# Kernel optimization log

Hardware: AMD Instinct MI355X
Metric: run time of the kernel (lower is better)

The kernel has to match this reference:

```python
import jax, jax.numpy as jnp
import numpy as np

B, T, H = 65536, 34, 64
T10_LO, T10_HI = 0.1, 5.0
M0_LO, M0_HI = 0.0, 10000.0


def setup_inputs() -> dict:
    key = jax.random.key(0)
    ks = jax.random.split(key, 24)
    sig = jax.random.uniform(ks[0], (B, T), jnp.float32, 0.1, 1.0)
    keep = jax.random.uniform(ks[1], (B, T)) > 0.3
    X_fa_in = jnp.where(keep, sig, 0.0)
    fa_vals = jax.random.uniform(ks[2], (B, T), jnp.float32, 0.05, 0.6)  # flip angles (rad)
    fa_mask = keep
    fa_len = jnp.sum(keep, axis=1).astype(jnp.int64)
    TR_vals = jax.random.uniform(ks[3], (B, 1), jnp.float32, 0.003, 0.01)
    gi = 1.0 / np.sqrt(H)
    p = {}
    p['gru_Wih'] = jax.random.uniform(ks[4], (3 * H, 2), jnp.float32, -gi, gi)
    p['gru_Whh'] = jax.random.uniform(ks[5], (3 * H, H), jnp.float32, -gi, gi)
    p['gru_bih'] = jax.random.uniform(ks[6], (3 * H,), jnp.float32, -gi, gi)
    p['gru_bhh'] = jax.random.uniform(ks[7], (3 * H,), jnp.float32, -gi, gi)
    p['score_T10_w'] = jax.random.normal(ks[8], (H,), jnp.float32) * gi
    p['score_M0_w'] = jax.random.normal(ks[9], (H,), jnp.float32) * gi
    def lin(kw, kb, fan_out, fan_in):
        b = 1.0 / np.sqrt(fan_in)
        return (jax.random.uniform(kw, (fan_out, fan_in), jnp.float32, -b, b),
                jax.random.uniform(kb, (fan_out,), jnp.float32, -b, b))
    p['regT_W1'], p['regT_b1'] = lin(ks[10], ks[11], 200, H)
    p['regT_W2'], p['regT_b2'] = lin(ks[12], ks[13], 200, 200)
    p['regT_W3'], p['regT_b3'] = lin(ks[14], ks[15], 1, 200)
    p['regM_W1'], p['regM_b1'] = lin(ks[16], ks[17], 200, H)
    p['regM_W2'], p['regM_b2'] = lin(ks[18], ks[19], 200, 200)
    p['regM_W3'], p['regM_b3'] = lin(ks[20], ks[21], 1, 200)
    return dict(X_fa_in=X_fa_in, fa_vals=fa_vals, fa_mask=fa_mask, fa_len=fa_len,
                TR_vals=TR_vals, **p)


def _forward_fill(X_fa_in, fa_vals):
    # Segmented last-observation-carried-forward via cummax of valid indices.
    valid = X_fa_in != 0
    idx = jnp.where(valid, jnp.arange(T)[None, :], -1)
    last = jax.lax.cummax(idx, axis=1)                     # [B,T] index of last nonzero
    g = jnp.clip(last, 0, T - 1)
    Xf = jnp.where(last >= 0, jnp.take_along_axis(X_fa_in, g, axis=1), 0.0)
    ff = jnp.where(last >= 0, jnp.take_along_axis(fa_vals, g, axis=1), 0.0)
    return Xf, ff


def _gru(x, Wih, Whh, bih, bhh):
    # x: [B,T,2] -> out: [B,T,H]; PyTorch GRU gate order (r, z, n)
    x_proj = jnp.einsum('btf,gf->btg', x, Wih) + bih       # [B,T,3H]
    def step(h, xp):
        gh = h @ Whh.T + bhh                               # [B,3H]
        xr, xz, xn = jnp.split(xp, 3, axis=-1)
        hr, hz, hn = jnp.split(gh, 3, axis=-1)
        r = jax.nn.sigmoid(xr + hr)
        z = jax.nn.sigmoid(xz + hz)
        n = jnp.tanh(xn + r * hn)
        h_new = (1.0 - z) * n + z * h
        return h_new, h_new
    h0 = jnp.zeros((x.shape[0], Whh.shape[1]), x.dtype)
    _, out = jax.lax.scan(step, h0, jnp.swapaxes(x_proj, 0, 1))
    return jnp.swapaxes(out, 0, 1)


def _mlp(h, W1, b1, W2, b2, W3, b3):
    # Dropout layers are identity in eval mode
    h = jax.nn.elu(h @ W1.T + b1)
    h = jax.nn.elu(h @ W2.T + b2)
    return h @ W3.T + b3


def reference(X_fa_in, fa_vals, fa_mask, fa_len, TR_vals,
              gru_Wih, gru_Whh, gru_bih, gru_bhh,
              score_T10_w, score_M0_w,
              regT_W1, regT_b1, regT_W2, regT_b2, regT_W3, regT_b3,
              regM_W1, regM_b1, regM_W2, regM_b2, regM_W3, regM_b3):
    Xf, ff = _forward_fill(X_fa_in, fa_vals)
    x = jnp.stack([Xf, ff], axis=-1)                       # [B,T,2]
    out = _gru(x, gru_Wih, gru_Whh, gru_bih, gru_bhh)      # [B,T,H]
    # attention pooling: softmax over time of a linear score
    sT = jax.nn.softmax(out @ score_T10_w, axis=1)[..., None]
    sM = jax.nn.softmax(out @ score_M0_w, axis=1)[..., None]
    hT = jnp.sum(out * sT, axis=1)                         # [B,H]
    hM = jnp.sum(out * sM, axis=1)
    T10_raw = _mlp(hT, regT_W1, regT_b1, regT_W2, regT_b2, regT_W3, regT_b3)[:, 0]
    M0_raw = _mlp(hM, regM_W1, regM_b1, regM_W2, regM_b2, regM_W3, regM_b3)[:, 0]
    T10 = T10_LO + jax.nn.sigmoid(T10_raw)[:, None] * (T10_HI - T10_LO)  # [B,1]
    M0 = M0_LO + jax.nn.sigmoid(M0_raw)[:, None] * (M0_HI - M0_LO)       # [B,1]
    R1 = 1.0 / T10
    E = jnp.exp(-TR_vals * R1)                             # [B,1]
    X_out = (1.0 - E) * jnp.sin(fa_vals) / (1.0 - jnp.cos(fa_vals) * E)  # [B,T]
    X_out = X_out * M0
    return (X_out, T10, M0)
```

## Files before the change

kernel.cpp:

```cpp
#include <hip/hip_runtime.h>

#define B_TOT 65536
#define T_LEN 34
#define HD 64
#define LOG2E 1.44269504088896340736f

typedef __attribute__((ext_vector_type(8))) short short8b;
typedef __attribute__((ext_vector_type(4))) short short4b;
typedef __attribute__((ext_vector_type(4))) float f32x4;
typedef __attribute__((ext_vector_type(4))) unsigned int u32x4;

__device__ __forceinline__ float frcp(float x){ return __builtin_amdgcn_rcpf(x); }
__device__ __forceinline__ float fexp2(float x){ return __builtin_amdgcn_exp2f(x); }
__device__ __forceinline__ float fsigmoid(float x){ return frcp(1.0f+__expf(-x)); }
__device__ __forceinline__ float felu(float x){ return x>0.0f ? x : (__expf(x)-1.0f); }

__device__ __forceinline__ unsigned short f2bf_rne(float f){
    unsigned int u = __float_as_uint(f);
    u += 0x7FFFu + ((u >> 16) & 1u);
    return (unsigned short)(u >> 16);
}
__device__ __forceinline__ float bf2f(unsigned short h){
    return __uint_as_float(((unsigned int)h) << 16);
}
__device__ __forceinline__ void split8(const float4& a, const float4& b,
                                       short8b& hi, short8b& lo){
    float f[8] = {a.x,a.y,a.z,a.w,b.x,b.y,b.z,b.w};
    #pragma unroll
    for (int i = 0; i < 8; ++i){
        unsigned short h = f2bf_rne(f[i]);
        hi[i] = (short)h;
        lo[i] = (short)f2bf_rne(f[i] - bf2f(h));
    }
}
__device__ __forceinline__ unsigned int cvt_pk_bf16(float lo, float hi){
    unsigned int r;
    asm("v_cvt_pk_bf16_f32 %0, %1, %2" : "=v"(r) : "v"(lo), "v"(hi));
    return r;
}
__device__ __forceinline__ int hswz(int r){ return ((r ^ (r >> 3)) & 7); }

__global__ __launch_bounds__(512)
void gru_attn_mfma(const float* __restrict__ Xin, const float* __restrict__ FA,
                   const float* __restrict__ Wih, const float* __restrict__ Whh,
                   const float* __restrict__ bih, const float* __restrict__ bhh,
                   const float* __restrict__ swT, const float* __restrict__ swM,
                   float* __restrict__ hT_out, float* __restrict__ hM_out)
{
    __shared__ __align__(16) unsigned short WF[28*512];
    __shared__ __align__(16) unsigned short HL[4][2][1024];
    __shared__ unsigned int XF[T_LEN*64];
    __shared__ __align__(8)  unsigned short XWc[12][16][4];

    const int tid  = threadIdx.x;
    const int lane = tid & 63;
    const int wv   = tid >> 6;
    const int l16  = lane & 15;
    const int lhi  = lane >> 4;
    const int wgru = wv & 3;
    const bool isPool = (wv >= 4);

    for (int f = wv; f < 28; f += 8) {
        unsigned short* dst = &WF[f*512 + lane*8];
        if (f < 24) {
            int ks = f / 12, nt = f % 12;
            int u_out = nt*16 + l16;
            float scale = (nt < 8) ? -LOG2E : 2.0f*LOG2E;
            #pragma unroll
            for (int j = 0; j < 8; ++j) {
                int k = ks*32 + lhi*8 + j;
                int u_in = (k & 3)*16 + (k >> 2);
                dst[j] = f2bf_rne(scale*Whh[u_out*64 + u_in]);
            }
        } else {
            int s = f - 24;
            const float* src = (s >= 2) ? swM : swT;
            int ks = s & 1;
            #pragma unroll
            for (int j = 0; j < 8; ++j) {
                int k = ks*32 + lhi*8 + j;
                int u_in = (k & 3)*16 + (k >> 2);
                dst[j] = f2bf_rne(LOG2E*src[u_in]);
            }
        }
    }
    if (tid < 192) {
        int nt  = tid >> 4;
        int u16 = tid & 15;
        int u_abs = (nt < 8) ? (nt*16 + u16) : (128 + (nt-8)*16 + u16);
        float s = (nt < 8) ? -LOG2E : 2.0f*LOG2E;
        float bias = (nt < 8) ? -LOG2E*(bih[u_abs] + bhh[u_abs])
                              : 2.0f*LOG2E*bih[u_abs];
        XWc[nt][u16][0] = f2bf_rne(s*Wih[u_abs*2]);
        XWc[nt][u16][1] = f2bf_rne(s*Wih[u_abs*2+1]);
        XWc[nt][u16][2] = f2bf_rne(bias);
        XWc[nt][u16][3] = 0;
    }
    for (int i = tid; i < 4*2*1024; i += 512)
        (&HL[0][0][0])[i] = 0;

    for (int i = 0; i < 8; ++i) {
        int brow = wv*8 + i;
        int row  = blockIdx.x*64 + brow;
        float X = 0.0f, fa = 0.0f; int idx = -1;
        if (lane < T_LEN) {
            X  = Xin[row*T_LEN + lane];
            fa = FA [row*T_LEN + lane];
            if (X != 0.0f) idx = lane;
        }
        #pragma unroll
        for (int off = 1; off < 64; off <<= 1) {
            int v = __shfl_up(idx, off);
            if (lane >= off && v > idx) idx = v;
        }
        int gsrc = idx < 0 ? 0 : idx;
        float Xg = __shfl(X,  gsrc);
        float fg = __shfl(fa, gsrc);
        if (idx < 0) { Xg = 0.0f; fg = 0.0f; }
        if (lane < T_LEN)
            XF[lane*64 + brow] =
                (unsigned int)f2bf_rne(Xg) | ((unsigned int)f2bf_rne(fg) << 16);
    }

    __syncthreads();

    const int sA    = hswz(l16) << 3;
    const int aoff0 = l16*64 + (( lhi   *8) ^ sA);
    const int aoff1 = l16*64 + (((4+lhi)*8) ^ sA);
    const f32x4 zero4 = (f32x4){0.f, 0.f, 0.f, 0.f};
    const unsigned short* WFl = &WF[lane*8];

    if (!isPool) {
        __builtin_amdgcn_s_setprio(1);
        const unsigned int extk2 = (lhi == 0) ? 0x00003f80u : 0u;
        const bool ext0 = (lhi == 0);
        const uint2* XWp = reinterpret_cast<const uint2*>(&XWc[0][0][0]);
        float biasN[4];
        #pragma unroll
        for (int g = 0; g < 4; ++g) biasN[g] = 2.0f*LOG2E*bhh[128 + g*16 + l16];

        float2 hreg2[4][2];
        #pragma unroll
        for (int q = 0; q < 4; ++q) { hreg2[q][0] = make_float2(0.f,0.f);
                                      hreg2[q][1] = make_float2(0.f,0.f); }

        for (int t = 0; t < T_LEN; ++t) {
            __syncthreads();
            const unsigned short* pb = &HL[wgru][(t+1)&1][0];
            unsigned short*       cb = &HL[wgru][ t   &1][0];
            short8b a0 = *reinterpret_cast<const short8b*>(&pb[aoff0]);
            short8b a1 = *reinterpret_cast<const short8b*>(&pb[aoff1]);
            unsigned int xw = XF[t*64 + wgru*16 + l16];
            u32x4 aeu = { ext0 ? xw : 0u, extk2, 0u, 0u };
            short8b aext = __builtin_bit_cast(short8b, aeu);

            #pragma unroll
            for (int g = 0; g < 4; ++g) {
                uint2 er = XWp[(g   )*16 + l16];
                uint2 ez = XWp[(4+g )*16 + l16];
                uint2 en = XWp[(8+g )*16 + l16];
                u32x4 bru = { ext0 ? er.x : 0u, ext0 ? er.y : 0u, 0u, 0u };
                u32x4 bzu = { ext0 ? ez.x : 0u, ext0 ? ez.y : 0u, 0u, 0u };
                u32x4 bnu = { ext0 ? en.x : 0u, ext0 ? en.y : 0u, 0u, 0u };

                f32x4 ar = __builtin_amdgcn_mfma_f32_16x16x32_bf16(
                    aext, __builtin_bit_cast(short8b, bru), zero4, 0,0,0);
                ar = __builtin_amdgcn_mfma_f32_16x16x32_bf16(
                    a0, *reinterpret_cast<const short8b*>(WFl + (g   )*512), ar, 0,0,0);
                ar = __builtin_amdgcn_mfma_f32_16x16x32_bf16(
                    a1, *reinterpret_cast<const short8b*>(WFl + (12+g)*512), ar, 0,0,0);
                f32x4 az = __builtin_amdgcn_mfma_f32_16x16x32_bf16(
                    aext, __builtin_bit_cast(short8b, bzu), zero4, 0,0,0);
                az = __builtin_amdgcn_mfma_f32_16x16x32_bf16(
                    a0, *reinterpret_cast<const short8b*>(WFl + (4+g )*512), az, 0,0,0);
                az = __builtin_amdgcn_mfma_f32_16x16x32_bf16(
                    a1, *reinterpret_cast<const short8b*>(WFl + (16+g)*512), az, 0,0,0);
                f32x4 anx = __builtin_amdgcn_mfma_f32_16x16x32_bf16(
                    aext, __builtin_bit_cast(short8b, bnu), zero4, 0,0,0);
                f32x4 anh = __builtin_amdgcn_mfma_f32_16x16x32_bf16(
                    a0, *reinterpret_cast<const short8b*>(WFl + (8+g )*512), zero4, 0,0,0);
                anh = __builtin_amdgcn_mfma_f32_16x16x32_bf16(
                    a1, *reinterpret_cast<const short8b*>(WFl + (20+g)*512), anh, 0,0,0);
                #pragma unroll
                for (int q = 0; q < 4; ++q) {
                    float r  = frcp(1.0f + fexp2(ar[q]));
                    float z  = frcp(1.0f + fexp2(az[q]));
                    float v  = fmaf(r, anh[q], fmaf(r, biasN[g], anx[q]));
                    float n  = fmaf(-2.0f, frcp(1.0f + fexp2(v)), 1.0f);
                    float h  = (g & 1) ? hreg2[q][g>>1].y : hreg2[q][g>>1].x;
                    float hn = fmaf(z, h - n, n);
                    if (g & 1) hreg2[q][g>>1].y = hn; else hreg2[q][g>>1].x = hn;
                }
            }
            #pragma unroll
            for (int q = 0; q < 4; ++q) {
                int rloc = lhi*4 + q;
                unsigned int d0 = cvt_pk_bf16(hreg2[q][0].x, hreg2[q][0].y);
                unsigned int d1 = cvt_pk_bf16(hreg2[q][1].x, hreg2[q][1].y);
                int so = rloc*64 + ((l16*4) ^ (hswz(rloc) << 3));
                *reinterpret_cast<uint2*>(&cb[so]) = make_uint2(d0, d1);
            }
        }
        __syncthreads();
    } else {
        float2 numT2[4][2], numM2[4][2];
        float  denT[4] = {}, denM[4] = {};
        #pragma unroll
        for (int q = 0; q < 4; ++q)
            #pragma unroll
            for (int j = 0; j < 2; ++j) {
                numT2[q][j] = make_float2(0.f, 0.f);
                numM2[q][j] = make_float2(0.f, 0.f);
            }

        for (int t = 0; t < T_LEN; ++t) {
            __syncthreads();
            if (t == 0) continue;
            const unsigned short* pb = &HL[wgru][(t+1)&1][0];
            short8b a0 = *reinterpret_cast<const short8b*>(&pb[aoff0]);
            short8b a1 = *reinterpret_cast<const short8b*>(&pb[aoff1]);
            f32x4 accT = __builtin_amdgcn_mfma_f32_16x16x32_bf16(
                a0, *reinterpret_cast<const short8b*>(WFl + 24*512), zero4, 0,0,0);
            accT = __builtin_amdgcn_mfma_f32_16x16x32_bf16(
                a1, *reinterpret_cast<const short8b*>(WFl + 25*512), accT, 0,0,0);
            f32x4 accM = __builtin_amdgcn_mfma_f32_16x16x32_bf16(
                a0, *reinterpret_cast<const short8b*>(WFl + 26*512), zero4, 0,0,0);
            accM = __builtin_amdgcn_mfma_f32_16x16x32_bf16(
                a1, *reinterpret_cast<const short8b*>(WFl + 27*512), accM, 0,0,0);
            #pragma unroll
            for (int q = 0; q < 4; ++q) {
                int rloc = lhi*4 + q;
                uint2 hq = *reinterpret_cast<const uint2*>(
                    &pb[rloc*64 + ((l16*4) ^ (hswz(rloc) << 3))]);
                float g0 = __uint_as_float(hq.x << 16);
                float g1 = __uint_as_float(hq.x & 0xFFFF0000u);
                float g2 = __uint_as_float(hq.y << 16);
                float g3 = __uint_as_float(hq.y & 0xFFFF0000u);
                float eT = fexp2(accT[q]);
                float eM = fexp2(accM[q]);
                denT[q] += eT; denM[q] += eM;
                numT2[q][0].x = fmaf(eT, g0, numT2[q][0].x);
                numT2[q][0].y = fmaf(eT, g1, numT2[q][0].y);
                numT2[q][1].x = fmaf(eT, g2, numT2[q][1].x);
                numT2[q][1].y = fmaf(eT, g3, numT2[q][1].y);
                numM2[q][0].x = fmaf(eM, g0, numM2[q][0].x);
                numM2[q][0].y = fmaf(eM, g1, numM2[q][0].y);
                numM2[q][1].x = fmaf(eM, g2, numM2[q][1].x);
                numM2[q][1].y = fmaf(eM, g3, numM2[q][1].y);
            }
        }
        __syncthreads();
        {
            const unsigned short* pb = &HL[wgru][1][0];
            short8b a0 = *reinterpret_cast<const short8b*>(&pb[aoff0]);
            short8b a1 = *reinterpret_cast<const short8b*>(&pb[aoff1]);
            f32x4 accT = __builtin_amdgcn_mfma_f32_16x16x32_bf16(
                a0, *reinterpret_cast<const short8b*>(WFl + 24*512), zero4, 0,0,0);
            accT = __builtin_amdgcn_mfma_f32_16x16x32_bf16(
                a1, *reinterpret_cast<const short8b*>(WFl + 25*512), accT, 0,0,0);
            f32x4 accM = __builtin_amdgcn_mfma_f32_16x16x32_bf16(
                a0, *reinterpret_cast<const short8b*>(WFl + 26*512), zero4, 0,0,0);
            accM = __builtin_amdgcn_mfma_f32_16x16x32_bf16(
                a1, *reinterpret_cast<const short8b*>(WFl + 27*512), accM, 0,0,0);
            #pragma unroll
            for (int q = 0; q < 4; ++q) {
                int rloc = lhi*4 + q;
                uint2 hq = *reinterpret_cast<const uint2*>(
                    &pb[rloc*64 + ((l16*4) ^ (hswz(rloc) << 3))]);
                float g0 = __uint_as_float(hq.x << 16);
                float g1 = __uint_as_float(hq.x & 0xFFFF0000u);
                float g2 = __uint_as_float(hq.y << 16);
                float g3 = __uint_as_float(hq.y & 0xFFFF0000u);
                float eT = fexp2(accT[q]);
                float eM = fexp2(accM[q]);
                denT[q] += eT; denM[q] += eM;
                numT2[q][0].x = fmaf(eT, g0, numT2[q][0].x);
                numT2[q][0].y = fmaf(eT, g1, numT2[q][0].y);
                numT2[q][1].x = fmaf(eT, g2, numT2[q][1].x);
                numT2[q][1].y = fmaf(eT, g3, numT2[q][1].y);
                numM2[q][0].x = fmaf(eM, g0, numM2[q][0].x);
                numM2[q][0].y = fmaf(eM, g1, numM2[q][0].y);
                numM2[q][1].x = fmaf(eM, g2, numM2[q][1].x);
                numM2[q][1].y = fmaf(eM, g3, numM2[q][1].y);
            }
        }
        const int rowbase = blockIdx.x*64 + wgru*16;
        #pragma unroll
        for (int q = 0; q < 4; ++q) {
            int row = rowbase + lhi*4 + q;
            float rT = frcp(denT[q]), rM = frcp(denM[q]);
            #pragma unroll
            for (int j = 0; j < 2; ++j) {
                hT_out[row*HD + (2*j  )*16 + l16] = numT2[q][j].x*rT;
                hT_out[row*HD + (2*j+1)*16 + l16] = numT2[q][j].y*rT;
                hM_out[row*HD + (2*j  )*16 + l16] = numM2[q][j].x*rM;
                hM_out[row*HD + (2*j+1)*16 + l16] = numM2[q][j].y*rM;
            }
        }
    }
}

__global__ __launch_bounds__(256)
void mlp_mfma(const float* __restrict__ hT, const float* __restrict__ hM,
    const float* __restrict__ TW1, const float* __restrict__ Tb1,
    const float* __restrict__ TW2, const float* __restrict__ Tb2,
    const float* __restrict__ TW3, const float* __restrict__ Tb3,
    const float* __restrict__ MW1, const float* __restrict__ Mb1,
    const float* __restrict__ MW2, const float* __restrict__ Mb2,
    const float* __restrict__ MW3, const float* __restrict__ Mb3,
    const float* __restrict__ FA, const float* __restrict__ TR,
    float* __restrict__ out)
{
    __shared__ __align__(16) unsigned short xh[2*64*64];
    __shared__ __align__(16) unsigned short h1s[64*256];
    __shared__ float praw[4][64];
    __shared__ float rawv[2][64];
    __shared__ float Es[64], M0s[64];

    const int tid  = threadIdx.x;
    const int lane = tid & 63;
    const int wv   = tid >> 6;
    const int l16  = lane & 15;
    const int lhi  = lane >> 4;
    const int row0 = blockIdx.x*64;

    {
        int r  = tid >> 2;
        int k0 = (tid & 3) * 16;
        int rx = r & 7;
        const float* pT = &hT[(row0+r)*64 + k0];
        const float* pM = &hM[(row0+r)*64 + k0];
        #pragma unroll
        for (int j = 0; j < 4; ++j) {
            float4 vT = *reinterpret_cast<const float4*>(pT + 4*j);
            float4 vM = *reinterpret_cast<const float4*>(pM + 4*j);
            int kk = k0 + 4*j;
            int ad = r*64 + ((((kk>>3) ^ rx))<<3) + (kk&7);
            short4b sT = { (short)f2bf_rne(vT.x), (short)f2bf_rne(vT.y),
                           (short)f2bf_rne(vT.z), (short)f2bf_rne(vT.w) };
            short4b sM = { (short)f2bf_rne(vM.x), (short)f2bf_rne(vM.y),
                           (short)f2bf_rne(vM.z), (short)f2bf_rne(vM.w) };
            *reinterpret_cast<short4b*>(&xh[ad])        = sT;
            *reinterpret_cast<short4b*>(&xh[4096 + ad]) = sM;
        }
        for (int i = tid; i < 64*24; i += 256) {
            int rr = i / 24, kk = 200 + i % 24;
            h1s[rr*256 + ((((kk>>3) ^ (rr&7)))<<3) + (kk&7)] = 0;
        }
    }
    __syncthreads();

    for (int brn = 0; brn < 2; ++brn) {
        const float* W1 = brn ? MW1 : TW1; const float* b1 = brn ? Mb1 : Tb1;
        const float* W2 = brn ? MW2 : TW2; const float* b2 = brn ? Mb2 : Tb2;
        const float* W3 = brn ? MW3 : TW3; const float* b3 = brn ? Mb3 : Tb3;

        for (int s = 0; s < 4; ++s) {
            int nt = wv + 4*s;
            if (nt > 12) break;
            int n  = nt*16 + l16;
            int nc = n < 200 ? n : 199;
            float bv = b1[nc];
            f32x4 acc[4];
            #pragma unroll
            for (int mt = 0; mt < 4; ++mt) acc[mt] = (f32x4){bv,bv,bv,bv};
            #pragma unroll
            for (int ks = 0; ks < 2; ++ks) {
                int k0 = ks*32 + lhi*8;
                const float* wp = &W1[nc*64 + k0];
                float4 w0 = *reinterpret_cast<const float4*>(wp);
                float4 w1 = *reinterpret_cast<const float4*>(wp + 4);
                short8b bh, bl;
                split8(w0, w1, bh, bl);
                #pragma unroll
                for (int mt = 0; mt < 4; ++mt) {
                    int rr = mt*16 + l16;
                    short8b a = *reinterpret_cast<const short8b*>(
                        &xh[brn*4096 + rr*64 + ((((k0>>3) ^ (rr&7)))<<3)]);
                    acc[mt] = __builtin_amdgcn_mfma_f32_16x16x32_bf16(a, bh, acc[mt], 0,0,0);
                    acc[mt] = __builtin_amdgcn_mfma_f32_16x16x32_bf16(a, bl, acc[mt], 0,0,0);
                }
            }
            if (n < 200) {
                #pragma unroll
                for (int mt = 0; mt < 4; ++mt) {
                    #pragma unroll
                    for (int q = 0; q < 4; ++q) {
                        int rr = mt*16 + lhi*4 + q;
                        h1s[rr*256 + ((((n>>3) ^ (rr&7)))<<3) + (n&7)] =
                            f2bf_rne(felu(acc[mt][q]));
                    }
                }
            }
        }
        __syncthreads();

        float p[4][4] = {};
        for (int s = 0; s < 4; ++s) {
            int nt = wv + 4*s;
            if (nt > 12) break;
            int n  = nt*16 + l16;
            int nc = n < 200 ? n : 199;
            float w3v = (n < 200) ? W3[nc] : 0.0f;
            float bv = b2[nc];
            f32x4 acc[4];
            #pragma unroll
            for (int mt = 0; mt < 4; ++mt) acc[mt] = (f32x4){bv,bv,bv,bv};
            for (int ks = 0; ks < 7; ++ks) {
                int k0 = ks*32 + lhi*8;
                short8b bh, bl;
                if (k0 + 8 <= 200) {
                    const float* wp = &W2[nc*200 + k0];
                    float4 w0 = *reinterpret_cast<const float4*>(wp);
                    float4 w1 = *reinterpret_cast<const float4*>(wp + 4);
                    split8(w0, w1, bh, bl);
                } else {
                    #pragma unroll
                    for (int i = 0; i < 8; ++i) { bh[i] = 0; bl[i] = 0; }
                }
                #pragma unroll
                for (int mt = 0; mt < 4; ++mt) {
                    int rr = mt*16 + l16;
                    short8b a = *reinterpret_cast<const short8b*>(
                        &h1s[rr*256 + ((((k0>>3) ^ (rr&7)))<<3)]);
                    acc[mt] = __builtin_amdgcn_mfma_f32_16x16x32_bf16(a, bh, acc[mt], 0,0,0);
                    acc[mt] = __builtin_amdgcn_mfma_f32_16x16x32_bf16(a, bl, acc[mt], 0,0,0);
                }
            }
            #pragma unroll
            for (int mt = 0; mt < 4; ++mt)
                #pragma unroll
                for (int q = 0; q < 4; ++q)
                    p[mt][q] = fmaf(w3v, felu(acc[mt][q]), p[mt][q]);
        }
        #pragma unroll
        for (int off = 1; off < 16; off <<= 1) {
            #pragma unroll
            for (int mt = 0; mt < 4; ++mt)
                #pragma unroll
                for (int q = 0; q < 4; ++q)
                    p[mt][q] += __shfl_xor(p[mt][q], off);
        }
        if (l16 == 0) {
            #pragma unroll
            for (int mt = 0; mt < 4; ++mt)
                #pragma unroll
                for (int q = 0; q < 4; ++q)
                    praw[wv][mt*16 + lhi*4 + q] = p[mt][q];
        }
        __syncthreads();
        if (tid < 64)
            rawv[brn][tid] = b3[0] + praw[0][tid] + praw[1][tid] + praw[2][tid] + praw[3][tid];
        __syncthreads();
    }

    if (tid < 64) {
        int row = row0 + tid;
        float T10 = 0.1f + 4.9f*fsigmoid(rawv[0][tid]);
        float M0  = 10000.0f*fsigmoid(rawv[1][tid]);
        Es[tid]  = __expf(-TR[row]/T10);
        M0s[tid] = M0;
        out[(size_t)B_TOT*T_LEN + row]         = T10;
        out[(size_t)B_TOT*T_LEN + B_TOT + row] = M0;
    }
    __syncthreads();
    for (int i = tid; i < 64*T_LEN; i += 256) {
        int rr = i / T_LEN, t = i - rr*T_LEN;
        int row = row0 + rr;
        float fa = FA[row*T_LEN + t];
        float s = __sinf(fa), c = __cosf(fa);
        float Ev = Es[rr];
        out[row*T_LEN + t] = (1.0f - Ev)*s*frcp(1.0f - c*Ev)*M0s[rr];
    }
}

extern "C" void kernel_launch(void* const* d_in, const int* in_sizes, int n_in,
                              void* d_out, int out_size, void* d_ws, size_t ws_size,
                              hipStream_t stream) {
    const float* Xin = (const float*)d_in[0];
    const float* FA  = (const float*)d_in[1];
    const float* TR  = (const float*)d_in[4];
    const float* Wih = (const float*)d_in[5];
    const float* Whh = (const float*)d_in[6];
    const float* bih = (const float*)d_in[7];
    const float* bhh = (const float*)d_in[8];
    const float* swT = (const float*)d_in[9];
    const float* swM = (const float*)d_in[10];
    const float* TW1 = (const float*)d_in[11]; const float* Tb1 = (const float*)d_in[12];
    const float* TW2 = (const float*)d_in[13]; const float* Tb2 = (const float*)d_in[14];
    const float* TW3 = (const float*)d_in[15]; const float* Tb3 = (const float*)d_in[16];
    const float* MW1 = (const float*)d_in[17]; const float* Mb1 = (const float*)d_in[18];
    const float* MW2 = (const float*)d_in[19]; const float* Mb2 = (const float*)d_in[20];
    const float* MW3 = (const float*)d_in[21]; const float* Mb3 = (const float*)d_in[22];
    float* out = (float*)d_out;

    float* hT = (float*)d_ws;
    float* hM = hT + (size_t)B_TOT*HD;

    gru_attn_mfma<<<B_TOT/64, 512, 0, stream>>>(Xin, FA, Wih, Whh, bih, bhh,
                                                swT, swM, hT, hM);
    mlp_mfma<<<B_TOT/64, 256, 0, stream>>>(hT, hM,
                                           TW1, Tb1, TW2, Tb2, TW3, Tb3,
                                           MW1, Mb1, MW2, Mb2, MW3, Mb3,
                                           FA, TR, out);
}
```

Baseline: 239.5 us.

## Split each GRU row-group across two waves by hidden-unit halves

```diff
diff --git a/kernel.cpp b/kernel.cpp
--- a/kernel.cpp
+++ b/kernel.cpp
@@ -40,7 +40,7 @@
 }
 __device__ __forceinline__ int hswz(int r){ return ((r ^ (r >> 3)) & 7); }
 
-__global__ __launch_bounds__(512)
+__global__ __launch_bounds__(768)
 void gru_attn_mfma(const float* __restrict__ Xin, const float* __restrict__ FA,
                    const float* __restrict__ Wih, const float* __restrict__ Whh,
                    const float* __restrict__ bih, const float* __restrict__ bhh,
@@ -57,10 +57,10 @@
     const int wv   = tid >> 6;
     const int l16  = lane & 15;
     const int lhi  = lane >> 4;
-    const int wgru = wv & 3;
-    const bool isPool = (wv >= 4);
-
-    for (int f = wv; f < 28; f += 8) {
+    const bool isPool = (wv >= 8);
+    const int grp  = isPool ? (wv - 8) : (wv >> 1);
+
+    for (int f = wv; f < 28; f += 12) {
         unsigned short* dst = &WF[f*512 + lane*8];
         if (f < 24) {
             int ks = f / 12, nt = f % 12;
@@ -96,12 +96,11 @@
         XWc[nt][u16][2] = f2bf_rne(bias);
         XWc[nt][u16][3] = 0;
     }
-    for (int i = tid; i < 4*2*1024; i += 512)
+    for (int i = tid; i < 4*2*1024; i += 768)
         (&HL[0][0][0])[i] = 0;
 
-    for (int i = 0; i < 8; ++i) {
-        int brow = wv*8 + i;
-        int row  = blockIdx.x*64 + brow;
+    for (int brow = wv; brow < 64; brow += 12) {
+        int row = blockIdx.x*64 + brow;
         float X = 0.0f, fa = 0.0f; int idx = -1;
         if (lane < T_LEN) {
             X  = Xin[row*T_LEN + lane];
@@ -132,30 +131,34 @@
 
     if (!isPool) {
         __builtin_amdgcn_s_setprio(1);
+        const int g0 = (wv & 1)*2;
         const unsigned int extk2 = (lhi == 0) ? 0x00003f80u : 0u;
         const bool ext0 = (lhi == 0);
         const uint2* XWp = reinterpret_cast<const uint2*>(&XWc[0][0][0]);
-        float biasN[4];
-        #pragma unroll
-        for (int g = 0; g < 4; ++g) biasN[g] = 2.0f*LOG2E*bhh[128 + g*16 + l16];
-
-        float2 hreg2[4][2];
-        #pragma unroll
-        for (int q = 0; q < 4; ++q) { hreg2[q][0] = make_float2(0.f,0.f);
-                                      hreg2[q][1] = make_float2(0.f,0.f); }
+        f32x4 biasN4[2];
+        #pragma unroll
+        for (int gg = 0; gg < 2; ++gg) {
+            float b = 2.0f*LOG2E*bhh[128 + (g0+gg)*16 + l16];
+            biasN4[gg] = (f32x4){b, b, b, b};
+        }
+
+        float2 hreg2[4];
+        #pragma unroll
+        for (int q = 0; q < 4; ++q) hreg2[q] = make_float2(0.f, 0.f);
 
         for (int t = 0; t < T_LEN; ++t) {
             __syncthreads();
-            const unsigned short* pb = &HL[wgru][(t+1)&1][0];
-            unsigned short*       cb = &HL[wgru][ t   &1][0];
+            const unsigned short* pb = &HL[grp][(t+1)&1][0];
+            unsigned short*       cb = &HL[grp][ t   &1][0];
             short8b a0 = *reinterpret_cast<const short8b*>(&pb[aoff0]);
             short8b a1 = *reinterpret_cast<const short8b*>(&pb[aoff1]);
-            unsigned int xw = XF[t*64 + wgru*16 + l16];
+            unsigned int xw = XF[t*64 + grp*16 + l16];
             u32x4 aeu = { ext0 ? xw : 0u, extk2, 0u, 0u };
             short8b aext = __builtin_bit_cast(short8b, aeu);
 
             #pragma unroll
-            for (int g = 0; g < 4; ++g) {
+            for (int gg = 0; gg < 2; ++gg) {
+                const int g = g0 + gg;
                 uint2 er = XWp[(g   )*16 + l16];
                 uint2 ez = XWp[(4+g )*16 + l16];
                 uint2 en = XWp[(8+g )*16 + l16];
@@ -178,27 +181,26 @@
                 f32x4 anx = __builtin_amdgcn_mfma_f32_16x16x32_bf16(
                     aext, __builtin_bit_cast(short8b, bnu), zero4, 0,0,0);
                 f32x4 anh = __builtin_amdgcn_mfma_f32_16x16x32_bf16(
-                    a0, *reinterpret_cast<const short8b*>(WFl + (8+g )*512), zero4, 0,0,0);
+                    a0, *reinterpret_cast<const short8b*>(WFl + (8+g )*512), biasN4[gg], 0,0,0);
                 anh = __builtin_amdgcn_mfma_f32_16x16x32_bf16(
                     a1, *reinterpret_cast<const short8b*>(WFl + (20+g)*512), anh, 0,0,0);
                 #pragma unroll
                 for (int q = 0; q < 4; ++q) {
                     float r  = frcp(1.0f + fexp2(ar[q]));
                     float z  = frcp(1.0f + fexp2(az[q]));
-                    float v  = fmaf(r, anh[q], fmaf(r, biasN[g], anx[q]));
+                    float v  = fmaf(r, anh[q], anx[q]);
                     float n  = fmaf(-2.0f, frcp(1.0f + fexp2(v)), 1.0f);
-                    float h  = (g & 1) ? hreg2[q][g>>1].y : hreg2[q][g>>1].x;
+                    float h  = gg ? hreg2[q].y : hreg2[q].x;
                     float hn = fmaf(z, h - n, n);
-                    if (g & 1) hreg2[q][g>>1].y = hn; else hreg2[q][g>>1].x = hn;
+                    if (gg) hreg2[q].y = hn; else hreg2[q].x = hn;
                 }
             }
             #pragma unroll
             for (int q = 0; q < 4; ++q) {
                 int rloc = lhi*4 + q;
-                unsigned int d0 = cvt_pk_bf16(hreg2[q][0].x, hreg2[q][0].y);
-                unsigned int d1 = cvt_pk_bf16(hreg2[q][1].x, hreg2[q][1].y);
-                int so = rloc*64 + ((l16*4) ^ (hswz(rloc) << 3));
-                *reinterpret_cast<uint2*>(&cb[so]) = make_uint2(d0, d1);
+                int so = rloc*64 + ((l16*4 + g0) ^ (hswz(rloc) << 3));
+                *reinterpret_cast<unsigned int*>(&cb[so]) =
+                    cvt_pk_bf16(hreg2[q].x, hreg2[q].y);
             }
         }
         __syncthreads();
@@ -216,7 +218,7 @@
         for (int t = 0; t < T_LEN; ++t) {
             __syncthreads();
             if (t == 0) continue;
-            const unsigned short* pb = &HL[wgru][(t+1)&1][0];
+            const unsigned short* pb = &HL[grp][(t+1)&1][0];
             short8b a0 = *reinterpret_cast<const short8b*>(&pb[aoff0]);
             short8b a1 = *reinterpret_cast<const short8b*>(&pb[aoff1]);
             f32x4 accT = __builtin_amdgcn_mfma_f32_16x16x32_bf16(
@@ -232,26 +234,26 @@
                 int rloc = lhi*4 + q;
                 uint2 hq = *reinterpret_cast<const uint2*>(
                     &pb[rloc*64 + ((l16*4) ^ (hswz(rloc) << 3))]);
-                float g0 = __uint_as_float(hq.x << 16);
-                float g1 = __uint_as_float(hq.x & 0xFFFF0000u);
-                float g2 = __uint_as_float(hq.y << 16);
-                float g3 = __uint_as_float(hq.y & 0xFFFF0000u);
+                float g0v = __uint_as_float(hq.x << 16);
+                float g1v = __uint_as_float(hq.x & 0xFFFF0000u);
+                float g2v = __uint_as_float(hq.y << 16);
+                float g3v = __uint_as_float(hq.y & 0xFFFF0000u);
                 float eT = fexp2(accT[q]);
                 float eM = fexp2(accM[q]);
                 denT[q] += eT; denM[q] += eM;
-                numT2[q][0].x = fmaf(eT, g0, numT2[q][0].x);
-                numT2[q][0].y = fmaf(eT, g1, numT2[q][0].y);
-                numT2[q][1].x = fmaf(eT, g2, numT2[q][1].x);
-                numT2[q][1].y = fmaf(eT, g3, numT2[q][1].y);
-                numM2[q][0].x = fmaf(eM, g0, numM2[q][0].x);
-                numM2[q][0].y = fmaf(eM, g1, numM2[q][0].y);
-                numM2[q][1].x = fmaf(eM, g2, numM2[q][1].x);
-                numM2[q][1].y = fmaf(eM, g3, numM2[q][1].y);
+                numT2[q][0].x = fmaf(eT, g0v, numT2[q][0].x);
+                numT2[q][0].y = fmaf(eT, g1v, numT2[q][0].y);
+                numT2[q][1].x = fmaf(eT, g2v, numT2[q][1].x);
+                numT2[q][1].y = fmaf(eT, g3v, numT2[q][1].y);
+                numM2[q][0].x = fmaf(eM, g0v, numM2[q][0].x);
+                numM2[q][0].y = fmaf(eM, g1v, numM2[q][0].y);
+                numM2[q][1].x = fmaf(eM, g2v, numM2[q][1].x);
+                numM2[q][1].y = fmaf(eM, g3v, numM2[q][1].y);
             }
         }
         __syncthreads();
         {
-            const unsigned short* pb = &HL[wgru][1][0];
+            const unsigned short* pb = &HL[grp][1][0];
             short8b a0 = *reinterpret_cast<const short8b*>(&pb[aoff0]);
             short8b a1 = *reinterpret_cast<const short8b*>(&pb[aoff1]);
             f32x4 accT = __builtin_amdgcn_mfma_f32_16x16x32_bf16(
@@ -267,24 +269,24 @@
                 int rloc = lhi*4 + q;
                 uint2 hq = *reinterpret_cast<const uint2*>(
                     &pb[rloc*64 + ((l16*4) ^ (hswz(rloc) << 3))]);
-                float g0 = __uint_as_float(hq.x << 16);
-                float g1 = __uint_as_float(hq.x & 0xFFFF0000u);
-                float g2 = __uint_as_float(hq.y << 16);
-                float g3 = __uint_as_float(hq.y & 0xFFFF0000u);
+                float g0v = __uint_as_float(hq.x << 16);
+                float g1v = __uint_as_float(hq.x & 0xFFFF0000u);
+                float g2v = __uint_as_float(hq.y << 16);
+                float g3v = __uint_as_float(hq.y & 0xFFFF0000u);
                 float eT = fexp2(accT[q]);
                 float eM = fexp2(accM[q]);
                 denT[q] += eT; denM[q] += eM;
-                numT2[q][0].x = fmaf(eT, g0, numT2[q][0].x);
-                numT2[q][0].y = fmaf(eT, g1, numT2[q][0].y);
-                numT2[q][1].x = fmaf(eT, g2, numT2[q][1].x);
-                numT2[q][1].y = fmaf(eT, g3, numT2[q][1].y);
-                numM2[q][0].x = fmaf(eM, g0, numM2[q][0].x);
-                numM2[q][0].y = fmaf(eM, g1, numM2[q][0].y);
-                numM2[q][1].x = fmaf(eM, g2, numM2[q][1].x);
-                numM2[q][1].y = fmaf(eM, g3, numM2[q][1].y);
-            }
-        }
-        const int rowbase = blockIdx.x*64 + wgru*16;
+                numT2[q][0].x = fmaf(eT, g0v, numT2[q][0].x);
+                numT2[q][0].y = fmaf(eT, g1v, numT2[q][0].y);
+                numT2[q][1].x = fmaf(eT, g2v, numT2[q][1].x);
+                numT2[q][1].y = fmaf(eT, g3v, numT2[q][1].y);
+                numM2[q][0].x = fmaf(eM, g0v, numM2[q][0].x);
+                numM2[q][0].y = fmaf(eM, g1v, numM2[q][0].y);
+                numM2[q][1].x = fmaf(eM, g2v, numM2[q][1].x);
+                numM2[q][1].y = fmaf(eM, g3v, numM2[q][1].y);
+            }
+        }
+        const int rowbase = blockIdx.x*64 + grp*16;
         #pragma unroll
         for (int q = 0; q < 4; ++q) {
             int row = rowbase + lhi*4 + q;
@@ -497,7 +499,7 @@
     float* hT = (float*)d_ws;
     float* hM = hT + (size_t)B_TOT*HD;
 
-    gru_attn_mfma<<<B_TOT/64, 512, 0, stream>>>(Xin, FA, Wih, Whh, bih, bhh,
+    gru_attn_mfma<<<B_TOT/64, 768, 0, stream>>>(Xin, FA, Wih, Whh, bih, bhh,
                                                 swT, swM, hT, hM);
     mlp_mfma<<<B_TOT/64, 256, 0, stream>>>(hT, hM,
                                            TW1, Tb1, TW2, Tb2, TW3, Tb3,
```

New measurement: 259.7 us. 1.08x slower.
